# Optimization experiments

Measured on AMD Instinct MI355X. Metric: run time of the kernel, lower is better.

The kernel has to match this reference:

```python
import jax, jax.numpy as jnp
import numpy as np

N, C, T, V, D = 128, 64, 256, 25, 64  # batch(*persons), in_ch, frames, joints, out_ch
RED = 4  # SE reduction


def _shift_indices(c, d, v):
    i = np.arange(v)[:, None]
    j = np.arange(c)[None, :]
    shift_in = ((i * c + j + j * c) % (c * v)).reshape(-1)
    jd = np.arange(d)[None, :]
    shift_out = ((i * d + jd - jd * d) % (d * v)).reshape(-1)
    return jnp.asarray(shift_in, jnp.int32), jnp.asarray(shift_out, jnp.int32)


def setup_inputs() -> dict:
    key = jax.random.key(0)
    ks = jax.random.split(key, 6)
    r = C // RED
    x0 = jax.random.normal(ks[0], (N, C, T, V), jnp.float32)
    fc1_w = jax.random.normal(ks[1], (r, C), jnp.float32) * (2.0 / C) ** 0.5
    fc1_b = jnp.zeros((r,), jnp.float32)
    fc2_w = jax.random.normal(ks[2], (4, r), jnp.float32) * (2.0 / r) ** 0.5
    fc2_b = jnp.zeros((4,), jnp.float32)
    W = jax.random.normal(ks[3], (4, C, D), jnp.float32) * (1.0 / D) ** 0.5
    b = jnp.zeros((4, D), jnp.float32)
    mask = jax.random.normal(ks[4], (1, V, C), jnp.float32) * 0.1  # Feature_Mask
    gamma = jnp.ones((V * D,), jnp.float32)
    beta = jnp.zeros((V * D,), jnp.float32)
    shift_in, shift_out = _shift_indices(C, D, V)
    return dict(x0=x0, epoch=100, fc1_w=fc1_w, fc1_b=fc1_b, fc2_w=fc2_w,
                fc2_b=fc2_b, W=W, b=b, mask=mask, gamma=gamma, beta=beta,
                shift_in=shift_in, shift_out=shift_out)


def reference(x0, epoch, fc1_w, fc1_b, fc2_w, fc2_b, W, b, mask, gamma, beta,
              shift_in, shift_out):
    n, c, t, v = x0.shape
    d = W.shape[-1]
    # DY_SEModule: global avg pool -> 1x1 conv -> relu -> 1x1 conv -> softmax(/tao)
    pooled = x0.mean(axis=(2, 3))                       # [n, c]
    h = jax.nn.relu(pooled @ fc1_w.T + fc1_b)           # [n, c//4]
    logits = h @ fc2_w.T + fc2_b                        # [n, 4]
    tao = 1.0 if epoch >= 60 else -(30.0 - 1.0) / 60.0 * epoch + 30.0
    gate = jax.nn.softmax(logits / tao, axis=1)         # [n, 4]
    # per-sample fused weights/bias
    Wf = jnp.einsum('kcd,nk->ncd', W, gate)             # [n, c, d]
    bf = jnp.einsum('kc,nk->nc', b, gate)               # [n, d]
    # shift-in gather + tanh feature mask
    x = x0.transpose(0, 2, 3, 1).reshape(n * t, v * c)  # [n*t, v*c]
    x = jnp.take(x, shift_in, axis=1).reshape(n * t, v, c)
    x = x * (jnp.tanh(mask) + 1.0)
    x = x.reshape(n, t, v, c)
    # per-sample linear
    x = jnp.einsum('ntvc,ncd->ntvd', x, Wf) + bf[:, None, None, :]
    # shift-out gather + BatchNorm1d over v*d features (training-mode stats)
    x = jnp.take(x.reshape(n * t, v * d), shift_out, axis=1)
    mu = x.mean(axis=0)
    var = x.var(axis=0)
    x = (x - mu) * jax.lax.rsqrt(var + 1e-5) * gamma + beta
    x = x.reshape(n, t, v, d).transpose(0, 3, 1, 2)     # [n, d, t, v]
    # residual (in==out -> identity down) + relu
    return jax.nn.relu(x + x0)
```

## Files before the change

kernel.cpp:

```cpp
#include <hip/hip_runtime.h>
#include <hip/hip_bf16.h>
#include <math.h>

#define N_   128
#define C_   64
#define T_   256
#define V_   25
#define D_   64
#define CTV  409600
#define TV   6400

typedef __attribute__((ext_vector_type(8))) short short8;
typedef __attribute__((ext_vector_type(4))) short short4v;
typedef __attribute__((ext_vector_type(4))) float f32x4;

__device__ inline unsigned short f2b(float f) {
    __hip_bfloat16 h = __float2bfloat16(f);
    return *(unsigned short*)&h;
}
__device__ inline float b2f(unsigned short u) {
    return __uint_as_float(((unsigned)u) << 16);
}

__global__ __launch_bounds__(256) void k_pool(const float* __restrict__ x0,
                                              float* __restrict__ pooled) {
    const int bid = blockIdx.x;
    const int tid = threadIdx.x;
    const float4* base = (const float4*)(x0 + (size_t)bid * TV);
    float s = 0.f;
    for (int i = tid; i < 1600; i += 256) {
        float4 f = base[i];
        s += (f.x + f.y) + (f.z + f.w);
    }
    #pragma unroll
    for (int off = 32; off > 0; off >>= 1) s += __shfl_down(s, off);
    __shared__ float red[4];
    if ((tid & 63) == 0) red[tid >> 6] = s;
    __syncthreads();
    if (tid == 0) pooled[bid] = (red[0] + red[1] + red[2] + red[3]) * (1.0f / TV);
}

__global__ __launch_bounds__(256) void k_se(
    const float* __restrict__ pooled, const float* __restrict__ fc1w,
    const float* __restrict__ fc1b,  const float* __restrict__ fc2w,
    const float* __restrict__ fc2b,  const float* __restrict__ Wm,
    const float* __restrict__ bm,    const float* __restrict__ mask,
    const int* __restrict__ shin,    const int* __restrict__ ep,
    unsigned short* __restrict__ Wfb, float* __restrict__ bfv,
    unsigned* __restrict__ gimg)
{
    __shared__ float sp[64], sh[16], sl[4];
    __shared__ float wk[64 * 65];
    const int tid = threadIdx.x, n = blockIdx.x;
    if (tid < 64) sp[tid] = pooled[n * 64 + tid];
    __syncthreads();
    if (tid < 16) {
        float s = fc1b[tid];
        #pragma unroll
        for (int c = 0; c < 64; c++) s = fmaf(sp[c], fc1w[tid * 64 + c], s);
        sh[tid] = fmaxf(s, 0.f);
    }
    __syncthreads();
    if (tid < 4) {
        float s = fc2b[tid];
        #pragma unroll
        for (int j = 0; j < 16; j++) s = fmaf(sh[j], fc2w[tid * 16 + j], s);
        sl[tid] = s;
    }
    __syncthreads();
    const int e = ep[0];
    const float tao = (e >= 60) ? 1.0f : (-(29.0f / 60.0f) * (float)e + 30.0f);
    const float it = 1.0f / tao;
    float l0 = sl[0] * it, l1 = sl[1] * it, l2 = sl[2] * it, l3 = sl[3] * it;
    float mx = fmaxf(fmaxf(l0, l1), fmaxf(l2, l3));
    float e0 = expf(l0 - mx), e1 = expf(l1 - mx), e2 = expf(l2 - mx), e3 = expf(l3 - mx);
    float inv = 1.0f / (e0 + e1 + e2 + e3);
    float ga[4] = {e0 * inv, e1 * inv, e2 * inv, e3 * inv};

    float accW[16];
    #pragma unroll
    for (int m = 0; m < 16; m++) accW[m] = 0.f;
    #pragma unroll
    for (int k = 0; k < 4; k++) {
        __syncthreads();
        for (int i = tid; i < 4096; i += 256)
            wk[(i >> 6) * 65 + (i & 63)] = Wm[k * 4096 + i];
        __syncthreads();
        #pragma unroll
        for (int m = 0; m < 16; m++) {
            int o = m * 256 + tid;
            int w  = o >> 10, s = (o >> 9) & 1;
            int ln = (o >> 3) & 63, j = o & 7;
            int c  = s * 32 + (ln >> 4) * 8 + j;
            int d  = w * 16 + (ln & 15);
            accW[m] = fmaf(ga[k], wk[c * 65 + d], accW[m]);
        }
    }
    #pragma unroll
    for (int m = 0; m < 16; m++)
        Wfb[(size_t)n * 4096 + m * 256 + tid] = f2b(accW[m]);
    if (tid < 64)
        bfv[n * 64 + tid] = ga[0] * bm[tid] + ga[1] * bm[64 + tid] +
                            ga[2] * bm[128 + tid] + ga[3] * bm[192 + tid];
    if (n == 0) {
        for (int j = tid; j < 1600; j += 256) {
            int s = shin[j];
            unsigned off = (unsigned)((s & 63) * 100 + (s >> 6));
            unsigned mgb = (unsigned)f2b(tanhf(mask[j]) + 1.0f);
            gimg[j] = (off << 16) | mgb;
        }
    }
}

__global__ __launch_bounds__(256, 4) void k_main(
    const float* __restrict__ x0, const unsigned short* __restrict__ Wfb,
    const float* __restrict__ bfv, const unsigned* __restrict__ gimg,
    __hip_bfloat16* __restrict__ y, float* __restrict__ sn)
{
    __shared__ unsigned short xs[6400];
    __shared__ unsigned short At[7616];
    __shared__ unsigned gimgS[1600];

    const int tid = threadIdx.x;
    const int w = tid >> 6, l = tid & 63, q = l >> 4, m = l & 15;
    const int n = blockIdx.x >> 4;
    const int tbase = (blockIdx.x & 15) * 16;

    short8 bf0 = *(const short8*)(Wfb + (size_t)n * 4096 + (w * 2 + 0) * 512 + l * 8);
    short8 bf1 = *(const short8*)(Wfb + (size_t)n * 4096 + (w * 2 + 1) * 512 + l * 8);
    const int d = w * 16 + m;
    const float bfl = bfv[n * 64 + d];

    for (int i = tid; i < 1600; i += 256) gimgS[i] = gimg[i];
    for (int i = tid; i < 408; i += 256) {
        int rr = i / 34, wo = i - rr * 34;
        int t = rr / 3, vr = rr - t * 3 + 1;
        ((unsigned*)At)[(96 + t * 4 + vr) * 34 + wo] = 0u;
    }

    float ss[25], sq[25];
    #pragma unroll
    for (int v = 0; v < 25; v++) { ss[v] = 0.f; sq[v] = 0.f; }

    for (int sub = 0; sub < 4; sub++) {
        const int t0 = tbase + sub * 4;
        __syncthreads();
        {
            const float4* src = (const float4*)x0;
            const int fb = n * 102400 + (t0 * 25) / 4;
            for (int i = tid; i < 1600; i += 256) {
                int c = i / 25, r = i - c * 25;
                float4 f = src[fb + c * 1600 + r];
                unsigned lo = ((unsigned)f2b(f.y) << 16) | f2b(f.x);
                unsigned hi = ((unsigned)f2b(f.w) << 16) | f2b(f.z);
                *(unsigned*)&xs[c * 100 + r * 4]     = lo;
                *(unsigned*)&xs[c * 100 + r * 4 + 2] = hi;
            }
        }
        __syncthreads();
        for (int p = tid; p < 3200; p += 256) {
            int cp = p & 31, rv = p >> 5;
            int t = rv / 25, v = rv - t * 25;
            int c = cp * 2;
            unsigned g0 = gimgS[v * 64 + c], g1 = gimgS[v * 64 + c + 1];
            float v0 = b2f(xs[(g0 >> 16) + t * 25]) * b2f((unsigned short)(g0 & 0xffff));
            float v1 = b2f(xs[(g1 >> 16) + t * 25]) * b2f((unsigned short)(g1 & 0xffff));
            int rho = (v >> 2) * 16 + t * 4 + (v & 3);
            *(unsigned*)&At[rho * 68 + c] = ((unsigned)f2b(v1) << 16) | f2b(v0);
        }
        __syncthreads();
        #pragma unroll
        for (int tau = 0; tau < 7; tau++) {
            const unsigned short* Ab = At + (tau * 16 + m) * 68 + q * 8;
            short4v a0l = *(const short4v*)(Ab);
            short4v a0h = *(const short4v*)(Ab + 4);
            short4v a1l = *(const short4v*)(Ab + 32);
            short4v a1h = *(const short4v*)(Ab + 36);
            short8 a0 = {a0l[0],a0l[1],a0l[2],a0l[3],a0h[0],a0h[1],a0h[2],a0h[3]};
            short8 a1 = {a1l[0],a1l[1],a1l[2],a1l[3],a1h[0],a1h[1],a1h[2],a1h[3]};
            f32x4 acc = {0.f, 0.f, 0.f, 0.f};
            acc = __builtin_amdgcn_mfma_f32_16x16x32_bf16(a0, bf0, acc, 0, 0, 0);
            acc = __builtin_amdgcn_mfma_f32_16x16x32_bf16(a1, bf1, acc, 0, 0, 0);
            const int t = t0 + q;
            __hip_bfloat16* yb = y + ((size_t)(n * T_ + t) * 25) * 64 + d;
            #pragma unroll
            for (int r = 0; r < 4; r++) {
                const int v = tau * 4 + r;
                if (v < 25) {
                    float val = acc[r] + bfl;
                    yb[v * 64] = __float2bfloat16(val);
                    ss[v] += val;
                    sq[v] = fmaf(val, val, sq[v]);
                }
            }
        }
    }
    #pragma unroll
    for (int v = 0; v < 25; v++) {
        ss[v] += __shfl_xor(ss[v], 16); ss[v] += __shfl_xor(ss[v], 32);
        sq[v] += __shfl_xor(sq[v], 16); sq[v] += __shfl_xor(sq[v], 32);
    }
    if (q == 0) {
        float* sb = sn + (size_t)n * 3200;
        #pragma unroll
        for (int v = 0; v < 25; v++) {
            atomicAdd(&sb[v * 64 + d], ss[v]);
            atomicAdd(&sb[1600 + v * 64 + d], sq[v]);
        }
    }
}

__global__ __launch_bounds__(256) void k_bn(
    const float* __restrict__ sn,
    const float* __restrict__ gamma, const float* __restrict__ beta,
    const int* __restrict__ shout,
    float* __restrict__ A2, float* __restrict__ B2, int* __restrict__ S2)
{
    int j = blockIdx.x * 256 + threadIdx.x;
    if (j >= 1600) return;
    int src = shout[j];
    float s = 0.f, qq = 0.f;
    for (int n = 0; n < 128; n++) {
        s  += sn[(size_t)n * 3200 + src];
        qq += sn[(size_t)n * 3200 + 1600 + src];
    }
    const float invn = 1.0f / 32768.0f;
    float mu = s * invn;
    float var = qq * invn - mu * mu;
    float rstd = rsqrtf(var + 1e-5f);
    float a = gamma[j] * rstd;
    float bb = beta[j] - mu * a;
    int dd = j & 63, vo = j >> 6;
    int jo = dd * 25 + vo;
    A2[jo] = a; B2[jo] = bb;
    S2[jo] = (src >> 6) * 66 + (src & 63);
}

__global__ __launch_bounds__(256) void k_out(
    const __hip_bfloat16* __restrict__ y, const float* __restrict__ x0,
    const float* __restrict__ A2, const float* __restrict__ B2,
    const int* __restrict__ S2, float* __restrict__ out)
{
    __shared__ __align__(16) unsigned short ys[8 * 1652];
    __shared__ float aS[1600], bS[1600];
    __shared__ int sS[1600];
    const int tid = threadIdx.x;
    const int n = blockIdx.x >> 5;
    const int t0 = (blockIdx.x & 31) * 8;
    const uint4* ysrc = (const uint4*)((const unsigned short*)y + (size_t)(n * T_ + t0) * 1600);
    for (int i = tid; i < 1600; i += 256) {
        uint4 g = ysrc[i];
        int tl = i / 200, r8 = (i - tl * 200) * 8;
        int v = r8 >> 6, d0 = r8 & 63;
        unsigned* p = (unsigned*)ys + ((tl * 1652 + v * 66 + d0) >> 1);
        p[0] = g.x; p[1] = g.y; p[2] = g.z; p[3] = g.w;
    }
    for (int i = tid; i < 1600; i += 256) { aS[i] = A2[i]; bS[i] = B2[i]; sS[i] = S2[i]; }
    __syncthreads();
    const float* xb = x0 + (size_t)n * CTV + t0 * 25;
    float* ob = out + (size_t)n * CTV + t0 * 25;
    for (int o = tid; o < 12800; o += 256) {
        int dd = o / 200, rem = o - dd * 200;
        int tl = rem / 25, vo = rem - tl * 25;
        int jo = dd * 25 + vo;
        float val = b2f(ys[tl * 1652 + sS[jo]]);
        int addr = dd * TV + rem;
        float r = fmaf(val, aS[jo], bS[jo]) + xb[addr];
        ob[addr] = fmaxf(r, 0.f);
    }
}

extern "C" void kernel_launch(void* const* d_in, const int* in_sizes, int n_in,
                              void* d_out, int out_size, void* d_ws, size_t ws_size,
                              hipStream_t stream) {
    const float* x0    = (const float*)d_in[0];
    const int*   ep    = (const int*)  d_in[1];
    const float* fc1w  = (const float*)d_in[2];
    const float* fc1b  = (const float*)d_in[3];
    const float* fc2w  = (const float*)d_in[4];
    const float* fc2b  = (const float*)d_in[5];
    const float* Wm    = (const float*)d_in[6];
    const float* bm    = (const float*)d_in[7];
    const float* mask  = (const float*)d_in[8];
    const float* gamma = (const float*)d_in[9];
    const float* beta  = (const float*)d_in[10];
    const int*   shin  = (const int*)  d_in[11];
    const int*   shout = (const int*)  d_in[12];
    float* out = (float*)d_out;

    float* wsf = (float*)d_ws;
    float*          pooled = wsf;
    float*          bfv    = wsf + 8192;
    unsigned*       gimg   = (unsigned*)(wsf + 16384);
    float*          A2     = wsf + 17984;
    float*          B2     = wsf + 19584;
    int*            S2     = (int*)(wsf + 21184);
    unsigned short* Wfb    = (unsigned short*)(wsf + 22784);
    float*          sn     = wsf + 284928;
    __hip_bfloat16* y      = (__hip_bfloat16*)(wsf + 694528);

    hipMemsetAsync(sn, 0, 409600 * sizeof(float), stream);
    k_pool<<<N_ * C_, 256, 0, stream>>>(x0, pooled);
    k_se<<<N_, 256, 0, stream>>>(pooled, fc1w, fc1b, fc2w, fc2b, Wm, bm, mask,
                                 shin, ep, Wfb, bfv, gimg);
    k_main<<<N_ * 16, 256, 0, stream>>>(x0, Wfb, bfv, gimg, y, sn);
    k_bn<<<7, 256, 0, stream>>>(sn, gamma, beta, shout, A2, B2, S2);
    k_out<<<N_ * 32, 256, 0, stream>>>(y, x0, A2, B2, S2, out);
}
```

Before: 653.9 us.

## Vectorize output epilogue, compute shift analytically, and parallelize BN reduction

k_out no longer stages per-feature scale, bias and gather-index tables in LDS. The shift-out source index is computed in closed form from dd and vo, and scale and bias are read as packed float2 values straight from global memory. Residual loads and output stores are widened to 4-float vectors, with nontemporal stores, and the kernel gets a launch-bounds occupancy hint. k_bn splits the 128-sample reduction across 4 lanes and combines them with shuffles, using more blocks. The closed-form shift hard-codes the specific shift_out pattern instead of reading the shout table, and the per-element ab reads go to global/cache instead of LDS.

```diff
diff --git a/kernel.cpp b/kernel.cpp
--- a/kernel.cpp
+++ b/kernel.cpp
@@ -214,36 +214,37 @@
     const float* __restrict__ sn,
     const float* __restrict__ gamma, const float* __restrict__ beta,
     const int* __restrict__ shout,
-    float* __restrict__ A2, float* __restrict__ B2, int* __restrict__ S2)
+    float2* __restrict__ ab)
 {
-    int j = blockIdx.x * 256 + threadIdx.x;
-    if (j >= 1600) return;
-    int src = shout[j];
+    const int tid = threadIdx.x;
+    const int jl = tid >> 2;
+    const int p  = tid & 3;
+    const int j = blockIdx.x * 64 + jl;
+    const int src = shout[j];
     float s = 0.f, qq = 0.f;
-    for (int n = 0; n < 128; n++) {
-        s  += sn[(size_t)n * 3200 + src];
-        qq += sn[(size_t)n * 3200 + 1600 + src];
-    }
-    const float invn = 1.0f / 32768.0f;
-    float mu = s * invn;
-    float var = qq * invn - mu * mu;
-    float rstd = rsqrtf(var + 1e-5f);
-    float a = gamma[j] * rstd;
-    float bb = beta[j] - mu * a;
-    int dd = j & 63, vo = j >> 6;
-    int jo = dd * 25 + vo;
-    A2[jo] = a; B2[jo] = bb;
-    S2[jo] = (src >> 6) * 66 + (src & 63);
-}
-
-__global__ __launch_bounds__(256) void k_out(
+    for (int nn = p; nn < 128; nn += 4) {
+        s  += sn[(size_t)nn * 3200 + src];
+        qq += sn[(size_t)nn * 3200 + 1600 + src];
+    }
+    s  += __shfl_xor(s, 1);  s  += __shfl_xor(s, 2);
+    qq += __shfl_xor(qq, 1); qq += __shfl_xor(qq, 2);
+    if (p == 0) {
+        const float invn = 1.0f / 32768.0f;
+        float mu = s * invn;
+        float var = qq * invn - mu * mu;
+        float rstd = rsqrtf(var + 1e-5f);
+        float a = gamma[j] * rstd;
+        float bb = beta[j] - mu * a;
+        int dd = j & 63, vo = j >> 6;
+        ab[dd * 25 + vo] = make_float2(a, bb);
+    }
+}
+
+__global__ __launch_bounds__(256, 6) void k_out(
     const __hip_bfloat16* __restrict__ y, const float* __restrict__ x0,
-    const float* __restrict__ A2, const float* __restrict__ B2,
-    const int* __restrict__ S2, float* __restrict__ out)
+    const float2* __restrict__ ab, float* __restrict__ out)
 {
     __shared__ __align__(16) unsigned short ys[8 * 1652];
-    __shared__ float aS[1600], bS[1600];
-    __shared__ int sS[1600];
     const int tid = threadIdx.x;
     const int n = blockIdx.x >> 5;
     const int t0 = (blockIdx.x & 31) * 8;
@@ -255,18 +256,28 @@
         unsigned* p = (unsigned*)ys + ((tl * 1652 + v * 66 + d0) >> 1);
         p[0] = g.x; p[1] = g.y; p[2] = g.z; p[3] = g.w;
     }
-    for (int i = tid; i < 1600; i += 256) { aS[i] = A2[i]; bS[i] = B2[i]; sS[i] = S2[i]; }
     __syncthreads();
     const float* xb = x0 + (size_t)n * CTV + t0 * 25;
     float* ob = out + (size_t)n * CTV + t0 * 25;
-    for (int o = tid; o < 12800; o += 256) {
-        int dd = o / 200, rem = o - dd * 200;
-        int tl = rem / 25, vo = rem - tl * 25;
-        int jo = dd * 25 + vo;
-        float val = b2f(ys[tl * 1652 + sS[jo]]);
-        int addr = dd * TV + rem;
-        float r = fmaf(val, aS[jo], bS[jo]) + xb[addr];
-        ob[addr] = fmaxf(r, 0.f);
+    for (int o4 = tid; o4 < 3200; o4 += 256) {
+        int dd = o4 / 50;
+        int rem4 = (o4 - dd * 50) * 4;
+        int ddm = dd;
+        if (ddm >= 25) ddm -= 25;
+        if (ddm >= 25) ddm -= 25;
+        int tl = rem4 / 25, vo = rem4 - tl * 25;
+        const int base = dd * TV + rem4;
+        f32x4 xv = *(const f32x4*)(xb + base);
+        f32x4 r;
+        #pragma unroll
+        for (int e = 0; e < 4; e++) {
+            int vy = vo - ddm; if (vy < 0) vy += 25;
+            float val = b2f(ys[tl * 1652 + vy * 66 + dd]);
+            float2 g = ab[dd * 25 + vo];
+            r[e] = fmaxf(fmaf(val, g.x, g.y) + xv[e], 0.f);
+            vo++; if (vo == 25) { vo = 0; tl++; }
+        }
+        __builtin_nontemporal_store(r, (f32x4*)(ob + base));
     }
 }
 
@@ -292,9 +303,7 @@
     float*          pooled = wsf;
     float*          bfv    = wsf + 8192;
     unsigned*       gimg   = (unsigned*)(wsf + 16384);
-    float*          A2     = wsf + 17984;
-    float*          B2     = wsf + 19584;
-    int*            S2     = (int*)(wsf + 21184);
+    float2*         ab     = (float2*)(wsf + 17984);
     unsigned short* Wfb    = (unsigned short*)(wsf + 22784);
     float*          sn     = wsf + 284928;
     __hip_bfloat16* y      = (__hip_bfloat16*)(wsf + 694528);
@@ -304,6 +313,6 @@
     k_se<<<N_, 256, 0, stream>>>(pooled, fc1w, fc1b, fc2w, fc2b, Wm, bm, mask,
                                  shin, ep, Wfb, bfv, gimg);
     k_main<<<N_ * 16, 256, 0, stream>>>(x0, Wfb, bfv, gimg, y, sn);
-    k_bn<<<7, 256, 0, stream>>>(sn, gamma, beta, shout, A2, B2, S2);
-    k_out<<<N_ * 32, 256, 0, stream>>>(y, x0, A2, B2, S2, out);
-}
+    k_bn<<<25, 256, 0, stream>>>(sn, gamma, beta, shout, ab);
+    k_out<<<N_ * 32, 256, 0, stream>>>(y, x0, ab, out);
+}
```

Measured after the change: 575.5 us. 12.0% less time.
